# Kernel tuning notes

Measured on AMD Instinct MI355X. Metric: run time of the kernel, lower is better.

Reference implementation:

```python
import jax, jax.numpy as jnp
import numpy as np

IN_DIM = 4096
OUT_DIM = 4096
RANK = 16
BATCH = 4
SEQ = 2048


def setup_inputs() -> dict:
    key = jax.random.key(0)
    ks = jax.random.split(key, 7)
    x = jax.random.normal(ks[0], (BATCH, SEQ, IN_DIM), dtype=jnp.float32)
    org_weight = jax.random.normal(ks[1], (OUT_DIM, IN_DIM), dtype=jnp.float32) * 0.02
    org_bias = jax.random.normal(ks[2], (OUT_DIM,), dtype=jnp.float32) * 0.02
    hada_w1_a = jax.random.normal(ks[3], (OUT_DIM, RANK), dtype=jnp.float32) * 0.1
    hada_w1_b = jax.random.normal(ks[4], (RANK, IN_DIM), dtype=jnp.float32)
    hada_w2_a = jax.random.normal(ks[5], (OUT_DIM, RANK), dtype=jnp.float32) * 0.1
    hada_w2_b = jax.random.normal(ks[6], (RANK, IN_DIM), dtype=jnp.float32)
    scalar = jnp.ones((), dtype=jnp.float32)
    return {
        "x": x,
        "org_weight": org_weight,
        "org_bias": org_bias,
        "hada_w1_a": hada_w1_a,
        "hada_w1_b": hada_w1_b,
        "hada_w2_a": hada_w2_a,
        "hada_w2_b": hada_w2_b,
        "scalar": scalar,
    }


def reference(x, org_weight, org_bias, hada_w1_a, hada_w1_b, hada_w2_a, hada_w2_b, scalar):
    scale = jnp.asarray(1.0, dtype=hada_w1_b.dtype)   # self.scale = 1.0
    multiplier = jnp.asarray(1.0, dtype=x.dtype)       # self.multiplier = 1.0
    # base = F.linear(x, org_weight, org_bias)
    base = jnp.einsum("bsi,oi->bso", x, org_weight) + org_bias
    # diff_weight = (w1a @ w1b) * (w2a @ w2b) * scale * scalar  -> [out, in]
    diff_weight = (hada_w1_a @ hada_w1_b) * (hada_w2_a @ hada_w2_b) * scale * scalar
    # delta = F.linear(x, diff_weight * multiplier)
    delta = jnp.einsum("bsi,oi->bso", x, diff_weight * multiplier)
    return base + delta
```

## Files before the change

kernel.cpp:

```cpp
#include <hip/hip_runtime.h>

#define IN_DIM 4096
#define OUT_DIM 4096
#define RANK 16
#define MDIM 8192

typedef unsigned short ushort_t;
typedef __attribute__((ext_vector_type(8))) short short8;
typedef __attribute__((ext_vector_type(4))) float floatx4;
typedef __attribute__((ext_vector_type(4))) ushort_t ushort4_t;
typedef __attribute__((ext_vector_type(2))) ushort_t ushort2_t;

__device__ __forceinline__ ushort_t f2b(float f) {
    union { float f; unsigned int i; } v; v.f = f;
    unsigned int u = v.i;
    u += 0x7FFFu + ((u >> 16) & 1u);
    return (ushort_t)(u >> 16);
}

#define GLOAD_LDS16(gp, lp)                                                    \
    __builtin_amdgcn_global_load_lds(                                          \
        (__attribute__((address_space(1))) void*)(gp),                         \
        (__attribute__((address_space(3))) void*)(lp), 16, 0, 0)

__global__ __launch_bounds__(256) void convx_kernel(
    const float4* __restrict__ x, ushort4_t* __restrict__ xb, int n4)
{
    int i = blockIdx.x * blockDim.x + threadIdx.x;
    int stride = gridDim.x * blockDim.x;
    for (; i < n4; i += stride) {
        float4 v = x[i];
        ushort4_t o;
        o.x = f2b(v.x); o.y = f2b(v.y); o.z = f2b(v.z); o.w = f2b(v.w);
        xb[i] = o;
    }
}

__global__ __launch_bounds__(256) void weff_kernel(
    const float* __restrict__ orgw,
    const float* __restrict__ w1a, const float* __restrict__ w1b,
    const float* __restrict__ w2a, const float* __restrict__ w2b,
    const float* __restrict__ scalar,
    ushort_t* __restrict__ weff)
{
    __shared__ float s1a[64 * RANK];
    __shared__ float s2a[64 * RANK];

    const int t  = threadIdx.x;
    const int i0 = blockIdx.x * 512 + t * 2;
    const int o0 = blockIdx.y * 64;

    for (int e = t; e < 64 * RANK; e += 256) {
        s1a[e] = w1a[o0 * RANK + e];
        s2a[e] = w2a[o0 * RANK + e];
    }

    float b1[RANK][2], b2[RANK][2];
    #pragma unroll
    for (int r = 0; r < RANK; ++r) {
        const float2 v1 = *(const float2*)&w1b[r * IN_DIM + i0];
        const float2 v2 = *(const float2*)&w2b[r * IN_DIM + i0];
        b1[r][0] = v1.x; b1[r][1] = v1.y;
        b2[r][0] = v2.x; b2[r][1] = v2.y;
    }
    __syncthreads();

    const float sc = scalar[0];
    for (int o = 0; o < 64; ++o) {
        float4 a1v[4], a2v[4];
        #pragma unroll
        for (int j = 0; j < 4; ++j) {
            a1v[j] = *(const float4*)&s1a[o * RANK + j * 4];
            a2v[j] = *(const float4*)&s2a[o * RANK + j * 4];
        }
        float p1_0 = 0.f, p1_1 = 0.f, p2_0 = 0.f, p2_1 = 0.f;
        #pragma unroll
        for (int j = 0; j < 4; ++j) {
            #pragma unroll
            for (int k = 0; k < 4; ++k) {
                const int r = j * 4 + k;
                const float a1 = (k == 0) ? a1v[j].x : (k == 1) ? a1v[j].y
                               : (k == 2) ? a1v[j].z : a1v[j].w;
                const float a2 = (k == 0) ? a2v[j].x : (k == 1) ? a2v[j].y
                               : (k == 2) ? a2v[j].z : a2v[j].w;
                p1_0 += a1 * b1[r][0]; p1_1 += a1 * b1[r][1];
                p2_0 += a2 * b2[r][0]; p2_1 += a2 * b2[r][1];
            }
        }
        const size_t idx = (size_t)(o0 + o) * IN_DIM + i0;
        const float2 ov = *(const float2*)&orgw[idx];
        ushort2_t st;
        st.x = f2b(ov.x + p1_0 * p2_0 * sc);
        st.y = f2b(ov.y + p1_1 * p2_1 * sc);
        *(ushort2_t*)&weff[idx] = st;
    }
}

#define BM 256
#define BN 256
#define BK 64

#define STAGE_A(buf, half, kcol)                                               \
    do {                                                                       \
        GLOAD_LDS16(gX0 + (size_t)(half) * (128 * IN_DIM) + (kcol),            \
                    (short*)&lA[buf][half][0][0] + w * 512);                   \
        GLOAD_LDS16(gX1 + (size_t)(half) * (128 * IN_DIM) + (kcol),            \
                    (short*)&lA[buf][half][0][0] + 4096 + w * 512);            \
    } while (0)

#define STAGE_B(buf, half, kcol)                                               \
    do {                                                                       \
        GLOAD_LDS16(gW0 + (size_t)(half) * (128 * IN_DIM) + (kcol),            \
                    (short*)&lB[buf][half][0][0] + w * 512);                   \
        GLOAD_LDS16(gW1 + (size_t)(half) * (128 * IN_DIM) + (kcol),            \
                    (short*)&lB[buf][half][0][0] + 4096 + w * 512);            \
    } while (0)

#define MFMA_(d, a, b) (d) = __builtin_amdgcn_mfma_f32_16x16x32_bf16((a), (b), (d), 0, 0, 0)

#define HALF_ITER(aB, bB, S1, S2, S3, S4)                                      \
    do {                                                                       \
        short8 a_lo[4][2], a_hi[4][2], b_lo[2][2], b_hi[2][2];                 \
        S1;                                                                    \
                           \
        _Pragma("unroll")                                                      \
        for (int mi = 0; mi < 4; ++mi) {                                       \
            a_lo[mi][0] = *(const short8*)((aB) + mi * 1024 + ok0);            \
            a_lo[mi][1] = *(const short8*)((aB) + mi * 1024 + ok1);            \
        }                                                                      \
        _Pragma("unroll")                                                      \
        for (int ni = 0; ni < 2; ++ni) {                                       \
            b_lo[ni][0] = *(const short8*)((bB) + ni * 1024 + ok0);            \
            b_lo[ni][1] = *(const short8*)((bB) + ni * 1024 + ok1);            \
        }                                                                      \
        asm volatile("" ::: "memory");                  \
                                     \
        _Pragma("unroll")                                                      \
        for (int mi = 0; mi < 4; ++mi) {                                       \
            a_hi[mi][0] = *(const short8*)((aB) + 4096 + mi * 1024 + ok0);     \
            a_hi[mi][1] = *(const short8*)((aB) + 4096 + mi * 1024 + ok1);     \
        }                                                                      \
        asm volatile("" ::: "memory");                  \
                                     \
        _Pragma("unroll")                                                      \
        for (int ni = 0; ni < 2; ++ni) {                                       \
            b_hi[ni][0] = *(const short8*)((bB) + 2048 + ni * 1024 + ok0);     \
            b_hi[ni][1] = *(const short8*)((bB) + 2048 + ni * 1024 + ok1);     \
        }                                                                      \
          \
        __builtin_amdgcn_s_barrier();                                          \
        asm volatile("s_waitcnt lgkmcnt(12)" ::: "memory");                    \
        __builtin_amdgcn_sched_barrier(0);                                     \
        __builtin_amdgcn_s_setprio(1);                                         \
        _Pragma("unroll")                                                      \
        for (int mi = 0; mi < 4; ++mi)                                         \
            _Pragma("unroll")                                                  \
            for (int ni = 0; ni < 2; ++ni) {                                   \
                MFMA_(acc[mi][ni], a_lo[mi][0], b_lo[ni][0]);                  \
                MFMA_(acc[mi][ni], a_lo[mi][1], b_lo[ni][1]);                  \
            }                                                                  \
        __builtin_amdgcn_s_setprio(0);                                         \
        __builtin_amdgcn_s_barrier();                                          \
                         \
        S2;                                                                    \
        __builtin_amdgcn_s_barrier();                                          \
        asm volatile("s_waitcnt lgkmcnt(4)" ::: "memory");                     \
        __builtin_amdgcn_sched_barrier(0);                                     \
        __builtin_amdgcn_s_setprio(1);                                         \
        _Pragma("unroll")                                                      \
        for (int mi = 0; mi < 4; ++mi)                                         \
            _Pragma("unroll")                                                  \
            for (int ni = 0; ni < 2; ++ni) {                                   \
                MFMA_(acc[4 + mi][ni], a_hi[mi][0], b_lo[ni][0]);              \
                MFMA_(acc[4 + mi][ni], a_hi[mi][1], b_lo[ni][1]);              \
            }                                                                  \
        __builtin_amdgcn_s_setprio(0);                                         \
        __builtin_amdgcn_s_barrier();                                          \
                                     \
        S3;                                                                    \
        __builtin_amdgcn_s_barrier();                                          \
        asm volatile("s_waitcnt lgkmcnt(0)" ::: "memory");                     \
        __builtin_amdgcn_sched_barrier(0);                                     \
        __builtin_amdgcn_s_setprio(1);                                         \
        _Pragma("unroll")                                                      \
        for (int mi = 0; mi < 4; ++mi)                                         \
            _Pragma("unroll")                                                  \
            for (int ni = 0; ni < 2; ++ni) {                                   \
                MFMA_(acc[4 + mi][2 + ni], a_hi[mi][0], b_hi[ni][0]);          \
                MFMA_(acc[4 + mi][2 + ni], a_hi[mi][1], b_hi[ni][1]);          \
            }                                                                  \
        __builtin_amdgcn_s_setprio(0);                                         \
        __builtin_amdgcn_s_barrier();                                          \
                  \
        S4;                                                                    \
        __builtin_amdgcn_s_barrier();                                          \
        __builtin_amdgcn_s_setprio(1);                                         \
        _Pragma("unroll")                                                      \
        for (int mi = 0; mi < 4; ++mi)                                         \
            _Pragma("unroll")                                                  \
            for (int ni = 0; ni < 2; ++ni) {                                   \
                MFMA_(acc[mi][2 + ni], a_lo[mi][0], b_hi[ni][0]);              \
                MFMA_(acc[mi][2 + ni], a_lo[mi][1], b_hi[ni][1]);              \
            }                                                                  \
        __builtin_amdgcn_s_setprio(0);                                         \
        asm volatile("s_waitcnt vmcnt(4)" ::: "memory");                       \
        __builtin_amdgcn_s_barrier();                                          \
    } while (0)

__global__ __launch_bounds__(512, 2) void gemm_kernel(
    const ushort_t* __restrict__ X,
    const ushort_t* __restrict__ W,
    const float* __restrict__ bias,
    float* __restrict__ out)
{
    __shared__ __align__(16) short lA[2][2][128][64];
    __shared__ __align__(16) short lB[2][2][128][64];

    const int t    = threadIdx.x;
    const int w    = t >> 6;
    const int lane = t & 63;
    const int quad = lane >> 4;
    const int r16  = lane & 15;
    const int wm   = w >> 2;
    const int wn   = w & 3;

    const int bid = blockIdx.y * gridDim.x + blockIdx.x;
    const int swz = (bid & 7) * 64 + (bid >> 3);
    const int m0  = (swz >> 4) * BM;
    const int n0  = (swz & 15) * BN;

    const int s0  = w * 64 + lane;
    const int s1  = 512 + s0;
    const int r0  = s0 >> 3, r1 = s1 >> 3;
    const int k80 = (s0 & 7) ^ (r0 & 7);
    const int k81 = (s1 & 7) ^ (r1 & 7);
    const ushort_t* gX0 = X + (size_t)(m0 + r0) * IN_DIM + k80 * 8;
    const ushort_t* gX1 = X + (size_t)(m0 + r1) * IN_DIM + k81 * 8;
    const ushort_t* gW0 = W + (size_t)(n0 + r0) * IN_DIM + k80 * 8;
    const ushort_t* gW1 = W + (size_t)(n0 + r1) * IN_DIM + k81 * 8;

    const short* aB0 = &lA[0][wm][r16][0];
    const short* aB1 = &lA[1][wm][r16][0];
    const short* bB0 = &lB[0][wn >> 1][(wn & 1) * 64 + r16][0];
    const short* bB1 = &lB[1][wn >> 1][(wn & 1) * 64 + r16][0];
    const int ok0 = ((0 + quad) ^ (r16 & 7)) << 3;
    const int ok1 = ((4 + quad) ^ (r16 & 7)) << 3;

    floatx4 acc[8][4];
    #pragma unroll
    for (int i = 0; i < 8; ++i)
        #pragma unroll
        for (int j = 0; j < 4; ++j)
            acc[i][j] = (floatx4){0.f, 0.f, 0.f, 0.f};

    STAGE_A(0, 0, 0);
    STAGE_A(0, 1, 0);
    STAGE_B(0, 0, 0);
    STAGE_B(0, 1, 0);
    STAGE_A(1, 0, 64);
    STAGE_A(1, 1, 64);
    asm volatile("s_waitcnt vmcnt(4)" ::: "memory");
    __builtin_amdgcn_s_barrier();

    for (int it = 0; it < IN_DIM / 128; ++it) {
        const int kmax = IN_DIM - 64;
        int kB1 = it * 128 + 64;  if (kB1 > kmax) kB1 = kmax;
        int kA2 = it * 128 + 128; if (kA2 > kmax) kA2 = kmax;
        int kA3 = it * 128 + 192; if (kA3 > kmax) kA3 = kmax;

        HALF_ITER(aB0, bB0,
                  STAGE_B(1, 0, kB1), STAGE_B(1, 1, kB1),
                  STAGE_A(0, 0, kA2), STAGE_A(0, 1, kA2));
        HALF_ITER(aB1, bB1,
                  STAGE_B(0, 0, kA2), STAGE_B(0, 1, kA2),
                  STAGE_A(1, 0, kA3), STAGE_A(1, 1, kA3));
    }

    #pragma unroll
    for (int ni = 0; ni < 4; ++ni) {
        const int gn = n0 + wn * 64 + ni * 16 + r16;
        const float bv = bias[gn];
        #pragma unroll
        for (int mi = 0; mi < 8; ++mi) {
            const int gm = m0 + wm * 128 + mi * 16 + quad * 4;
            #pragma unroll
            for (int rr = 0; rr < 4; ++rr)
                out[(size_t)(gm + rr) * OUT_DIM + gn] = acc[mi][ni][rr] + bv;
        }
    }
}

extern "C" void kernel_launch(void* const* d_in, const int* in_sizes, int n_in,
                              void* d_out, int out_size, void* d_ws, size_t ws_size,
                              hipStream_t stream) {
    const float* x      = (const float*)d_in[0];
    const float* orgw   = (const float*)d_in[1];
    const float* bias   = (const float*)d_in[2];
    const float* w1a    = (const float*)d_in[3];
    const float* w1b    = (const float*)d_in[4];
    const float* w2a    = (const float*)d_in[5];
    const float* w2b    = (const float*)d_in[6];
    const float* scalar = (const float*)d_in[7];

    ushort_t* xb   = (ushort_t*)d_ws;
    ushort_t* weff = (ushort_t*)d_ws + (size_t)MDIM * IN_DIM;
    float* out = (float*)d_out;

    const int n4 = MDIM * IN_DIM / 4;
    convx_kernel<<<2048, 256, 0, stream>>>((const float4*)x, (ushort4_t*)xb, n4);
    weff_kernel<<<dim3(IN_DIM / 512, OUT_DIM / 64), 256, 0, stream>>>(
        orgw, w1a, w1b, w2a, w2b, scalar, weff);
    gemm_kernel<<<dim3(OUT_DIM / BN, MDIM / BM), 512, 0, stream>>>(
        xb, weff, bias, out);
}
```

Measured before the change: 630.0 us.

## Prefetch next tile's first LDS fragments across half-iterations and swap A/B staging order

Restructures the GEMM main loop so the first group of LDS fragment reads for the next k-tile is issued during the last MFMA quadrant of the current one. LDS reads are split into smaller groups interleaved with the MFMA quadrants, and the quadrant order changes. The global-to-LDS staging order now stages B ahead and A behind, with adjusted waitcnt values. The aim is to hide LDS read latency and keep the matrix units busy, at the cost of more live registers and tighter synchronisation that could introduce hazards.

After: 644.3 us. 2.3% more time.

```diff
diff --git a/kernel.cpp b/kernel.cpp
--- a/kernel.cpp
+++ b/kernel.cpp
@@ -118,11 +118,8 @@
 
 #define MFMA_(d, a, b) (d) = __builtin_amdgcn_mfma_f32_16x16x32_bf16((a), (b), (d), 0, 0, 0)
 
-#define HALF_ITER(aB, bB, S1, S2, S3, S4)                                      \
-    do {                                                                       \
-        short8 a_lo[4][2], a_hi[4][2], b_lo[2][2], b_hi[2][2];                 \
-        S1;                                                                    \
-                           \
+#define READ_G1(aB, bB)                                                        \
+    do {                                                                       \
         _Pragma("unroll")                                                      \
         for (int mi = 0; mi < 4; ++mi) {                                       \
             a_lo[mi][0] = *(const short8*)((aB) + mi * 1024 + ok0);            \
@@ -133,77 +130,90 @@
             b_lo[ni][0] = *(const short8*)((bB) + ni * 1024 + ok0);            \
             b_lo[ni][1] = *(const short8*)((bB) + ni * 1024 + ok1);            \
         }                                                                      \
-        asm volatile("" ::: "memory");                  \
-                                     \
-        _Pragma("unroll")                                                      \
-        for (int mi = 0; mi < 4; ++mi) {                                       \
-            a_hi[mi][0] = *(const short8*)((aB) + 4096 + mi * 1024 + ok0);     \
-            a_hi[mi][1] = *(const short8*)((aB) + 4096 + mi * 1024 + ok1);     \
-        }                                                                      \
-        asm volatile("" ::: "memory");                  \
-                                     \
+    } while (0)
+
+#define READ_G2(bB)                                                            \
+    do {                                                                       \
         _Pragma("unroll")                                                      \
         for (int ni = 0; ni < 2; ++ni) {                                       \
             b_hi[ni][0] = *(const short8*)((bB) + 2048 + ni * 1024 + ok0);     \
             b_hi[ni][1] = *(const short8*)((bB) + 2048 + ni * 1024 + ok1);     \
         }                                                                      \
-          \
-        __builtin_amdgcn_s_barrier();                                          \
-        asm volatile("s_waitcnt lgkmcnt(12)" ::: "memory");                    \
-        __builtin_amdgcn_sched_barrier(0);                                     \
-        __builtin_amdgcn_s_setprio(1);                                         \
+    } while (0)
+
+#define READ_G3A(aB)                                                           \
+    do {                                                                       \
+        _Pragma("unroll")                                                      \
+        for (int mi = 0; mi < 2; ++mi) {                                       \
+            a_hi[mi][0] = *(const short8*)((aB) + 4096 + mi * 1024 + ok0);     \
+            a_hi[mi][1] = *(const short8*)((aB) + 4096 + mi * 1024 + ok1);     \
+        }                                                                      \
+    } while (0)
+
+#define READ_G3B(aB)                                                           \
+    do {                                                                       \
+        _Pragma("unroll")                                                      \
+        for (int mi = 2; mi < 4; ++mi) {                                       \
+            a_hi[mi][0] = *(const short8*)((aB) + 4096 + mi * 1024 + ok0);     \
+            a_hi[mi][1] = *(const short8*)((aB) + 4096 + mi * 1024 + ok1);     \
+        }                                                                      \
+    } while (0)
+
+#define Q_MFMA(mb, nb, afr, bfr)                                               \
+    do {                                                                       \
         _Pragma("unroll")                                                      \
         for (int mi = 0; mi < 4; ++mi)                                         \
             _Pragma("unroll")                                                  \
             for (int ni = 0; ni < 2; ++ni) {                                   \
-                MFMA_(acc[mi][ni], a_lo[mi][0], b_lo[ni][0]);                  \
-                MFMA_(acc[mi][ni], a_lo[mi][1], b_lo[ni][1]);                  \
+                MFMA_(acc[(mb) + mi][(nb) + ni], afr[mi][0], bfr[ni][0]);      \
+                MFMA_(acc[(mb) + mi][(nb) + ni], afr[mi][1], bfr[ni][1]);      \
             }                                                                  \
+    } while (0)
+
+#define HALF_ITER(aBc, bBc, aBn, bBn, SS1, SS2, SS3, SS4)                      \
+    do {                                                                       \
+                                                                       \
+        READ_G2(bBc);                                                          \
+        READ_G3A(aBc);                                                         \
+        __builtin_amdgcn_sched_barrier(0);                                     \
+        SS1;                                                                   \
+        __builtin_amdgcn_s_barrier();                                          \
+        asm volatile("s_waitcnt lgkmcnt(8)" ::: "memory");                     \
+        __builtin_amdgcn_sched_barrier(0);                                     \
+        __builtin_amdgcn_s_setprio(1);                                         \
+        Q_MFMA(0, 0, a_lo, b_lo);                                              \
         __builtin_amdgcn_s_setprio(0);                                         \
         __builtin_amdgcn_s_barrier();                                          \
-                         \
-        S2;                                                                    \
-        __builtin_amdgcn_s_barrier();                                          \
-        asm volatile("s_waitcnt lgkmcnt(4)" ::: "memory");                     \
+                                                                       \
+        READ_G3B(aBc);                                                         \
+        __builtin_amdgcn_sched_barrier(0);                                     \
+        SS2;                                                                   \
+        __builtin_amdgcn_s_barrier();                                          \
+        asm volatile("s_waitcnt lgkmcnt(8)" ::: "memory");                     \
         __builtin_amdgcn_sched_barrier(0);                                     \
         __builtin_amdgcn_s_setprio(1);                                         \
-        _Pragma("unroll")                                                      \
-        for (int mi = 0; mi < 4; ++mi)                                         \
-            _Pragma("unroll")                                                  \
-            for (int ni = 0; ni < 2; ++ni) {                                   \
-                MFMA_(acc[4 + mi][ni], a_hi[mi][0], b_lo[ni][0]);              \
-                MFMA_(acc[4 + mi][ni], a_hi[mi][1], b_lo[ni][1]);              \
-            }                                                                  \
+        Q_MFMA(0, 2, a_lo, b_hi);                                              \
         __builtin_amdgcn_s_setprio(0);                                         \
         __builtin_amdgcn_s_barrier();                                          \
-                                     \
-        S3;                                                                    \
+                                                                       \
+        SS3;                                                                   \
         __builtin_amdgcn_s_barrier();                                          \
         asm volatile("s_waitcnt lgkmcnt(0)" ::: "memory");                     \
         __builtin_amdgcn_sched_barrier(0);                                     \
         __builtin_amdgcn_s_setprio(1);                                         \
-        _Pragma("unroll")                                                      \
-        for (int mi = 0; mi < 4; ++mi)                                         \
-            _Pragma("unroll")                                                  \
-            for (int ni = 0; ni < 2; ++ni) {                                   \
-                MFMA_(acc[4 + mi][2 + ni], a_hi[mi][0], b_hi[ni][0]);          \
-                MFMA_(acc[4 + mi][2 + ni], a_hi[mi][1], b_hi[ni][1]);          \
-            }                                                                  \
+        Q_MFMA(4, 0, a_hi, b_lo);                                              \
         __builtin_amdgcn_s_setprio(0);                                         \
+        asm volatile("s_waitcnt vmcnt(2)" ::: "memory");                       \
         __builtin_amdgcn_s_barrier();                                          \
                   \
-        S4;                                                                    \
-        __builtin_amdgcn_s_barrier();                                          \
+        READ_G1(aBn, bBn);                                                     \
+        __builtin_amdgcn_sched_barrier(0);                                     \
+        SS4;                                                                   \
+        __builtin_amdgcn_s_barrier();                                          \
+        __builtin_amdgcn_sched_barrier(0);                                     \
         __builtin_amdgcn_s_setprio(1);                                         \
-        _Pragma("unroll")                                                      \
-        for (int mi = 0; mi < 4; ++mi)                                         \
-            _Pragma("unroll")                                                  \
-            for (int ni = 0; ni < 2; ++ni) {                                   \
-                MFMA_(acc[mi][2 + ni], a_lo[mi][0], b_hi[ni][0]);              \
-                MFMA_(acc[mi][2 + ni], a_lo[mi][1], b_hi[ni][1]);              \
-            }                                                                  \
+        Q_MFMA(4, 2, a_hi, b_hi);                                              \
         __builtin_amdgcn_s_setprio(0);                                         \
-        asm volatile("s_waitcnt vmcnt(4)" ::: "memory");                       \
         __builtin_amdgcn_s_barrier();                                          \
     } while (0)
 
@@ -253,27 +263,31 @@
         for (int j = 0; j < 4; ++j)
             acc[i][j] = (floatx4){0.f, 0.f, 0.f, 0.f};
 
+    short8 a_lo[4][2], a_hi[4][2], b_lo[2][2], b_hi[2][2];
+
     STAGE_A(0, 0, 0);
     STAGE_A(0, 1, 0);
     STAGE_B(0, 0, 0);
     STAGE_B(0, 1, 0);
-    STAGE_A(1, 0, 64);
-    STAGE_A(1, 1, 64);
+    STAGE_B(1, 0, 64);
+    STAGE_B(1, 1, 64);
     asm volatile("s_waitcnt vmcnt(4)" ::: "memory");
     __builtin_amdgcn_s_barrier();
+    READ_G1(aB0, bB0);
+    __builtin_amdgcn_sched_barrier(0);
 
     for (int it = 0; it < IN_DIM / 128; ++it) {
         const int kmax = IN_DIM - 64;
-        int kB1 = it * 128 + 64;  if (kB1 > kmax) kB1 = kmax;
-        int kA2 = it * 128 + 128; if (kA2 > kmax) kA2 = kmax;
-        int kA3 = it * 128 + 192; if (kA3 > kmax) kA3 = kmax;
-
-        HALF_ITER(aB0, bB0,
-                  STAGE_B(1, 0, kB1), STAGE_B(1, 1, kB1),
-                  STAGE_A(0, 0, kA2), STAGE_A(0, 1, kA2));
-        HALF_ITER(aB1, bB1,
-                  STAGE_B(0, 0, kA2), STAGE_B(0, 1, kA2),
-                  STAGE_A(1, 0, kA3), STAGE_A(1, 1, kA3));
+        int kA1 = it * 128 + 64;  if (kA1 > kmax) kA1 = kmax;
+        int kB2 = it * 128 + 128; if (kB2 > kmax) kB2 = kmax;
+        int kB3 = it * 128 + 192; if (kB3 > kmax) kB3 = kmax;
+
+        HALF_ITER(aB0, bB0, aB1, bB1,
+                  STAGE_A(1, 0, kA1), STAGE_A(1, 1, kA1),
+                  STAGE_B(0, 0, kB2), STAGE_B(0, 1, kB2));
+        HALF_ITER(aB1, bB1, aB0, bB0,
+                  STAGE_A(0, 0, kB2), STAGE_A(0, 1, kB2),
+                  STAGE_B(1, 0, kB3), STAGE_B(1, 1, kB3));
     }
 
     #pragma unroll
```
